# Kernel optimization log

Measured on AMD Instinct MI355X. Metric: run time of the kernel, lower is better.

The kernel has to match this reference:

```python
import jax, jax.numpy as jnp
import numpy as np

PAD_TOKEN = 0.0
REPLACEMENT_PROB = 0.1


def setup_inputs() -> dict:
    key = jax.random.key(0)
    # item-ID-like values in [0, 100000); zeros act as pad tokens
    x = jax.random.randint(key, (16384, 2048), 0, 100000).astype(jnp.float32)
    return {"x": x}


def reference(x):
    """Stochastic Swap Noise: replace ~p of non-pad positions with values
    sampled without replacement from the non-pad values of the tensor.

    Jit-friendly equivalent of torch's
      bernoulli -> masked_select compaction -> randperm -> scatter
    chain: a single argsort on random keys (pads keyed to +2.0) both
    compacts the non-pad values to the front AND shuffles them; a cumsum
    over the replacement mask assigns each replaced position its donor.
    """
    key = jax.random.key(42)
    k_bern, k_shuf = jax.random.split(key)

    nonpad = x != PAD_TOKEN                                        # [B,S] bool
    repl = (jax.random.uniform(k_bern, x.shape) < REPLACEMENT_PROB) & nonpad

    flat_x = x.reshape(-1)                                          # [N]
    flat_nonpad = nonpad.reshape(-1)
    flat_repl = repl.reshape(-1)

    # compaction + shuffle in one sort: non-pad elems get uniform [0,1) keys,
    # pads get 2.0 so they sink to the end.
    r = jnp.where(flat_nonpad, jax.random.uniform(k_shuf, flat_x.shape), 2.0)
    order = jnp.argsort(r)
    donors = flat_x[order]                                          # shuffled non-pad values first

    # k-th replaced position (in flat order) takes donors[k]
    rank = jnp.cumsum(flat_repl) - 1                                # -1 where not replaced (masked out below)
    out = jnp.where(flat_repl, donors[rank], flat_x)
    return out.reshape(x.shape)
```

## Files before the change

kernel.cpp:

```cpp
#include <hip/hip_runtime.h>
#include <stdint.h>

static __host__ __device__ inline uint32_t rotl32(uint32_t x, int r) {
#if defined(__HIP_DEVICE_COMPILE__)
  return __builtin_amdgcn_alignbit(x, x, (uint32_t)(32 - r));
#else
  return (x << r) | (x >> (32 - r));
#endif
}

static __host__ __device__ inline void tf2x32(uint32_t k0, uint32_t k1,
                                              uint32_t x0, uint32_t x1,
                                              uint32_t& o0, uint32_t& o1) {
  uint32_t k2 = k0 ^ k1 ^ 0x1BD11BDAu;
#define TFR(a) { x0 += x1; x1 = rotl32(x1, a); x1 ^= x0; }
  x0 += k0; x1 += k1;
  TFR(13) TFR(15) TFR(26) TFR(6)
  x0 += k1; x1 += k2 + 1u;
  TFR(17) TFR(29) TFR(16) TFR(24)
  x0 += k2; x1 += k0 + 2u;
  TFR(13) TFR(15) TFR(26) TFR(6)
  x0 += k0; x1 += k1 + 3u;
  TFR(17) TFR(29) TFR(16) TFR(24)
  x0 += k1; x1 += k2 + 4u;
  TFR(13) TFR(15) TFR(26) TFR(6)
  x0 += k2; x1 += k0 + 5u;
#undef TFR
  o0 = x0; o1 = x1;
}

static __device__ inline uint32_t fold_bits(uint32_t k0, uint32_t k1, uint32_t ctr) {
  uint32_t a, b;
  tf2x32(k0, k1, 0u, ctr, a, b);
  return a ^ b;
}

#define CUT2      917504u
#define NBINS2    1792u
#define NH        2048
#define ELEMS_G   8192
#define GPOOL     1216u
#define BSCAP     2432u
#define WIN       4096
#define CAPDUMP   3932160u
#define STRIDE    2432u
#define MASKI     0x07FFFFFFu
#define BERN_THR  838861u



template<bool BOUNDS>
__global__ __launch_bounds__(256) void k_gen(const float* __restrict__ x,
                                             uint64_t* __restrict__ mask,
                                             uint32_t* __restrict__ rsums,
                                             uint32_t* __restrict__ dumpCursor,
                                             uint2* __restrict__ dump,
                                             uint32_t bk0, uint32_t bk1,
                                             uint32_t sk0, uint32_t sk1, int n) {
  __shared__ uint2 pool[GPOOL];
  __shared__ uint32_t wcnt[4];
  __shared__ uint32_t lpoolCnt, lgbase;
  int tid = threadIdx.x, lane = tid & 63, wid = tid >> 6;
  int base = blockIdx.x * ELEMS_G;
  if (tid == 0) lpoolCnt = 0;
  __syncthreads();

  uint32_t cnt = 0;
  uint64_t lt = (1ull << lane) - 1ull;
  unsigned long long bball[4];
  for (int it = 0; it < ELEMS_G / 1024; it++) {
    int e0 = base + it * 1024 + wid * 256 + lane * 4;
    float4 xv;
    if (!BOUNDS || e0 + 3 < n) {
      xv = *reinterpret_cast<const float4*>(x + e0);
    } else {
      xv.x = (e0 + 0 < n) ? x[e0 + 0] : 0.0f;
      xv.y = (e0 + 1 < n) ? x[e0 + 1] : 0.0f;
      xv.z = (e0 + 2 < n) ? x[e0 + 2] : 0.0f;
      xv.w = (e0 + 3 < n) ? x[e0 + 3] : 0.0f;
    }
#define GENE(e, comp)                                                     \
    {                                                                     \
      uint32_t ii = (uint32_t)(e0 + e);                                   \
      bool np = (comp != 0.0f);                                           \
      uint32_t bb = fold_bits(bk0, bk1, ii);                              \
      bool rr = np && ((bb >> 9) < BERN_THR);                             \
      bball[e] = __ballot(rr);                                            \
      uint32_t mm = fold_bits(sk0, sk1, ii) >> 9;                         \
      bool cand = np && (mm < CUT2);                                      \
      unsigned long long cb = __ballot(cand);                             \
      uint32_t pb = 0;                                                    \
      if (lane == 0 && cb) pb = atomicAdd(&lpoolCnt, (uint32_t)__popcll(cb)); \
      pb = __builtin_amdgcn_readfirstlane(pb);                            \
      if (cand) {                                                         \
        uint32_t slot = pb + (uint32_t)__popcll(cb & lt);                 \
        if (slot < GPOOL) {                                               \
          uint32_t v = (uint32_t)comp;                                    \
          pool[slot] = make_uint2((mm << 12) | (v >> 5),                  \
                                  ((v & 31u) << 27) | ii);                \
        }                                                                 \
      }                                                                   \
    }
    GENE(0, xv.x) GENE(1, xv.y) GENE(2, xv.z) GENE(3, xv.w)
#undef GENE
    cnt += (uint32_t)(__popcll(bball[0]) + __popcll(bball[1]) +
                      __popcll(bball[2]) + __popcll(bball[3]));
    if (lane == 0) {
      uint32_t ci = (uint32_t)blockIdx.x * 32u + (uint32_t)it * 4u + (uint32_t)wid;
      if (!BOUNDS) {
        mask[ci * 4 + 0] = bball[0]; mask[ci * 4 + 1] = bball[1];
        mask[ci * 4 + 2] = bball[2]; mask[ci * 4 + 3] = bball[3];
      } else {
        for (int e = 0; e < 4; e++)
          if ((int)(ci * 256u + (uint32_t)e * 64u) < n) mask[ci * 4 + e] = bball[e];
      }
    }
  }
  if (lane == 0) wcnt[wid] = cnt;
  __syncthreads();
  if (tid == 0) {
    rsums[blockIdx.x] = wcnt[0] + wcnt[1] + wcnt[2] + wcnt[3];
    uint32_t pc = lpoolCnt; if (pc > GPOOL) pc = GPOOL;
    lgbase = atomicAdd((unsigned int*)dumpCursor, pc);
  }
  __syncthreads();
  uint32_t pc = lpoolCnt; if (pc > GPOOL) pc = GPOOL;
  uint32_t gb = lgbase;
  for (uint32_t j = tid; j < pc; j += 256) {
    uint32_t d = gb + j;
    if (d < CAPDUMP) dump[d] = pool[j];
  }
}

__global__ void k_scan2(uint32_t* __restrict__ data0, int n0,
                        uint32_t* __restrict__ data1, int n1) {
  __shared__ uint32_t wsum[4];
  uint32_t* data = (blockIdx.x == 0) ? data0 : data1;
  int n = (blockIdx.x == 0) ? n0 : n1;
  int tid = threadIdx.x, lane = tid & 63, wid = tid >> 6;
  uint32_t running = 0;
  for (int base = 0; base < n; base += 256) {
    int i = base + tid;
    uint32_t v = (i < n) ? data[i] : 0u;
    uint32_t incl = v;
    for (int d = 1; d < 64; d <<= 1) {
      uint32_t t = __shfl_up(incl, (unsigned)d, 64);
      if (lane >= d) incl += t;
    }
    if (lane == 63) wsum[wid] = incl;
    __syncthreads();
    uint32_t woff = 0, tot = 0;
    for (int w = 0; w < 4; w++) { uint32_t s = wsum[w]; if (w < wid) woff += s; tot += s; }
    if (i < n) data[i] = running + woff + (incl - v);
    running += tot;
    __syncthreads();
  }
  if (tid == 0) data[n] = running;
}

__global__ __launch_bounds__(256) void k_regroup(const uint2* __restrict__ dump,
                                                 const uint32_t* __restrict__ dumpCursor,
                                                 uint32_t* __restrict__ fineCursor,
                                                 uint2* __restrict__ fine) {
  __shared__ uint2    pool2[WIN];
  __shared__ uint32_t lhist[NH];
  __shared__ uint32_t lgbase[NH];
  __shared__ uint32_t wsums[4];
  int tid = threadIdx.x, lane = tid & 63, wid = tid >> 6;
  uint32_t total = dumpCursor[0];
  if (total > CAPDUMP) total = CAPDUMP;
  uint32_t wbase = blockIdx.x * (uint32_t)WIN;
  if (wbase >= total) return;
  uint32_t valid = total - wbase;
  if (valid > WIN) valid = WIN;

  for (int b = tid; b < NH; b += 256) lhist[b] = 0;
  __syncthreads();
  uint2 e[WIN / 256];
#pragma unroll
  for (int q = 0; q < WIN / 256; q++) {
    uint32_t j = (uint32_t)q * 256u + (uint32_t)tid;
    e[q] = (j < valid) ? dump[wbase + j] : make_uint2(0u, 0u);
    if (j < valid) atomicAdd(&lhist[e[q].x >> 21], 1u);
  }
  __syncthreads();
  for (int b = tid; b < NH; b += 256) {
    uint32_t h = lhist[b];
    lgbase[b] = h ? atomicAdd((unsigned int*)&fineCursor[b], h) : 0u;
  }
  __syncthreads();
  uint32_t hv[8], tsum = 0;
#pragma unroll
  for (int j = 0; j < 8; j++) { hv[j] = lhist[8 * tid + j]; tsum += hv[j]; }
  uint32_t incl = tsum;
  for (int d = 1; d < 64; d <<= 1) {
    uint32_t t = __shfl_up(incl, (unsigned)d, 64);
    if (lane >= d) incl += t;
  }
  if (lane == 63) wsums[wid] = incl;
  __syncthreads();
  if (wid == 0) {
    uint32_t v = (lane < 4) ? wsums[lane] : 0u;
    uint32_t in2 = v;
    for (int d = 1; d < 4; d <<= 1) {
      uint32_t t = __shfl_up(in2, (unsigned)d, 64);
      if (lane >= d) in2 += t;
    }
    if (lane < 4) wsums[lane] = in2 - v;
  }
  __syncthreads();
  uint32_t run = wsums[wid] + (incl - tsum);
#pragma unroll
  for (int j = 0; j < 8; j++) { uint32_t h = hv[j]; lhist[8 * tid + j] = run; run += h; }
  __syncthreads();
#pragma unroll
  for (int q = 0; q < WIN / 256; q++) {
    uint32_t j = (uint32_t)q * 256u + (uint32_t)tid;
    if (j < valid) {
      uint32_t b = e[q].x >> 21;
      uint32_t lpos = atomicAdd(&lhist[b], 1u);
      pool2[lpos] = e[q];
    }
  }
  __syncthreads();
  for (uint32_t j = tid; j < valid; j += 256) {
    uint2 p = pool2[j];
    uint32_t b = p.x >> 21;
    uint32_t st = (b == 0) ? 0u : lhist[b - 1];
    uint32_t dst = lgbase[b] + (j - st);
    if (dst < STRIDE) fine[(size_t)b * STRIDE + dst] = p;
  }
}

__global__ __launch_bounds__(256) void k_binsort(const uint2* __restrict__ pairs,
                                                 const uint32_t* __restrict__ binPrefix,
                                                 float* __restrict__ donors) {
  __shared__ uint2    lbuf[BSCAP];
  __shared__ uint32_t hist[512];
  __shared__ uint32_t wsums[4];
  int tid = threadIdx.x, lane = tid & 63, wid = tid >> 6;
  uint32_t bin = blockIdx.x;
  uint32_t gbase = binPrefix[bin];
  uint32_t cnt = binPrefix[bin + 1] - gbase;
  if (cnt > STRIDE) cnt = STRIDE;
  if (cnt > BSCAP) cnt = BSCAP;
  const uint2* src = pairs + (size_t)bin * STRIDE;

  for (int c = tid; c < 512; c += 256) hist[c] = 0;
  __syncthreads();
  for (uint32_t j = tid; j < cnt; j += 256)
    atomicAdd(&hist[(src[j].x >> 12) & 511u], 1u);
  __syncthreads();
  uint32_t h0 = hist[2 * tid], h1 = hist[2 * tid + 1];
  uint32_t tsum = h0 + h1;
  uint32_t incl = tsum;
  for (int d = 1; d < 64; d <<= 1) {
    uint32_t t = __shfl_up(incl, (unsigned)d, 64);
    if (lane >= d) incl += t;
  }
  if (lane == 63) wsums[wid] = incl;
  __syncthreads();
  if (wid == 0) {
    uint32_t v = (lane < 4) ? wsums[lane] : 0u;
    uint32_t in2 = v;
    for (int d = 1; d < 4; d <<= 1) {
      uint32_t t = __shfl_up(in2, (unsigned)d, 64);
      if (lane >= d) in2 += t;
    }
    if (lane < 4) wsums[lane] = in2 - v;
  }
  __syncthreads();
  uint32_t texcl = wsums[wid] + (incl - tsum);
  uint32_t e0 = texcl, e1 = e0 + h0;
  __syncthreads();
  hist[2 * tid] = e0; hist[2 * tid + 1] = e1;
  __syncthreads();
  for (uint32_t j = tid; j < cnt; j += 256) {
    uint2 p = src[j];
    uint32_t c = (p.x >> 12) & 511u;
    uint32_t lpos = atomicAdd(&hist[c], 1u);
    lbuf[lpos] = p;
  }
  __syncthreads();
  for (int c = tid; c < 512; c += 256) {
    uint32_t lo = (c == 0) ? 0u : hist[c - 1];
    uint32_t hi = hist[c];
    for (uint32_t u = lo + 1; u < hi; u++) {
      uint2 v = lbuf[u];
      uint32_t w = u;
      while (w > lo && (lbuf[w - 1].y & MASKI) > (v.y & MASKI)) {
        lbuf[w] = lbuf[w - 1];
        w--;
      }
      lbuf[w] = v;
    }
  }
  __syncthreads();
  for (uint32_t j = tid; j < cnt; j += 256) {
    uint2 p = lbuf[j];
    uint32_t v = ((p.x & 0xFFFu) << 5) | (p.y >> 27);
    donors[gbase + j] = (float)v;
  }
}

template<bool BOUNDS>
__global__ __launch_bounds__(256) void k_final(const float* __restrict__ x,
                                               const uint64_t* __restrict__ mask,
                                               const uint32_t* __restrict__ rsums,
                                               const float* __restrict__ donors,
                                               float* __restrict__ out, int n) {
  __shared__ uint64_t lw[ELEMS_G / 64];
  __shared__ uint32_t ctot[32], cpre[32];
  int tid = threadIdx.x, lane = tid & 63, wid = tid >> 6;
  int base = blockIdx.x * ELEMS_G;
  int wordBase = blockIdx.x * (ELEMS_G / 64);
  if (tid < ELEMS_G / 64) {
    uint64_t w = 0ull;
    int wI = wordBase + tid;
    if (!BOUNDS || (((wI >> 2) * 256) + ((wI & 3) * 64) < n)) w = mask[wI];
    lw[tid] = w;
  }
  __syncthreads();
  if (tid < 32) {
    ctot[tid] = (uint32_t)(__popcll(lw[4 * tid]) + __popcll(lw[4 * tid + 1]) +
                           __popcll(lw[4 * tid + 2]) + __popcll(lw[4 * tid + 3]));
  }
  __syncthreads();
  if (tid == 0) {
    uint32_t run = 0;
    for (int c = 0; c < 32; c++) { cpre[c] = run; run += ctot[c]; }
  }
  __syncthreads();
  uint32_t rbase = rsums[blockIdx.x];
  uint64_t lt = (1ull << lane) - 1ull;
  for (int it = 0; it < ELEMS_G / 1024; it++) {
    int c = it * 4 + wid;
    uint64_t b0 = lw[c * 4 + 0], b1 = lw[c * 4 + 1],
             b2 = lw[c * 4 + 2], b3 = lw[c * 4 + 3];
    uint32_t running = rbase + cpre[c];
    int e0 = base + it * 1024 + wid * 256 + lane * 4;
    uint32_t below = (uint32_t)(__popcll(b0 & lt) + __popcll(b1 & lt) +
                                __popcll(b2 & lt) + __popcll(b3 & lt));
    uint32_t r0 = (uint32_t)((b0 >> lane) & 1ull), r1 = (uint32_t)((b1 >> lane) & 1ull);
    uint32_t r2 = (uint32_t)((b2 >> lane) & 1ull), r3 = (uint32_t)((b3 >> lane) & 1ull);
    uint32_t rk = running + below;
    float4 xv;
    if (!BOUNDS || e0 + 3 < n) {
      xv = *reinterpret_cast<const float4*>(x + e0);
    } else {
      xv.x = (e0 + 0 < n) ? x[e0 + 0] : 0.0f;
      xv.y = (e0 + 1 < n) ? x[e0 + 1] : 0.0f;
      xv.z = (e0 + 2 < n) ? x[e0 + 2] : 0.0f;
      xv.w = (e0 + 3 < n) ? x[e0 + 3] : 0.0f;
    }
    float4 ov;
    ov.x = r0 ? donors[rk] : xv.x;               rk += r0;
    ov.y = r1 ? donors[rk] : xv.y;               rk += r1;
    ov.z = r2 ? donors[rk] : xv.z;               rk += r2;
    ov.w = r3 ? donors[rk] : xv.w;
    if (!BOUNDS || e0 + 3 < n) {
      *reinterpret_cast<float4*>(out + e0) = ov;
    } else {
      if (e0 + 0 < n) out[e0 + 0] = ov.x;
      if (e0 + 1 < n) out[e0 + 1] = ov.y;
      if (e0 + 2 < n) out[e0 + 2] = ov.z;
      if (e0 + 3 < n) out[e0 + 3] = ov.w;
    }
  }
}

extern "C" void kernel_launch(void* const* d_in, const int* in_sizes, int n_in,
                              void* d_out, int out_size, void* d_ws, size_t ws_size,
                              hipStream_t stream) {
  const float* x = (const float*)d_in[0];
  float* out = (float*)d_out;
  int n = in_sizes[0];
  (void)n_in; (void)out_size; (void)ws_size;

  uint32_t bk0, bk1, sk0, sk1;
  tf2x32(0u, 42u, 0u, 0u, bk0, bk1);
  tf2x32(0u, 42u, 0u, 1u, sk0, sk1);

  int nBlkG = (n + ELEMS_G - 1) / ELEMS_G;
  bool exact = ((n % ELEMS_G) == 0);

  size_t off = 0;
  auto alloc = [&](size_t bytes) -> void* {
    void* p = (uint8_t*)d_ws + off;
    off += (bytes + 255) & ~(size_t)255;
    return p;
  };
  uint32_t* dumpCursor = (uint32_t*)alloc(4);
  uint32_t* fineCursor = (uint32_t*)alloc((size_t)(NH + 1) * 4);
  size_t zeroBytes = off;
  uint32_t* rsums      = (uint32_t*)alloc((size_t)(nBlkG + 1) * 4);
  uint64_t* mask       = (uint64_t*)alloc((size_t)((n + 63) / 64 + 4) * 8);
  uint2*    dump       = (uint2*)alloc((size_t)CAPDUMP * 8);
  uint2*    fine       = (uint2*)alloc((size_t)NBINS2 * STRIDE * 8);
  float*    donors     = (float*)dump;

  hipMemsetAsync(d_ws, 0, zeroBytes, stream);

  if (exact)
    k_gen<false><<<nBlkG, 256, 0, stream>>>(x, mask, rsums, dumpCursor, dump,
                                            bk0, bk1, sk0, sk1, n);
  else
    k_gen<true><<<nBlkG, 256, 0, stream>>>(x, mask, rsums, dumpCursor, dump,
                                           bk0, bk1, sk0, sk1, n);
  int nWin = (int)((CAPDUMP + WIN - 1) / WIN);
  k_regroup<<<nWin, 256, 0, stream>>>(dump, dumpCursor, fineCursor, fine);
  k_scan2<<<2, 256, 0, stream>>>(rsums, nBlkG, fineCursor, (int)NBINS2);
  k_binsort<<<(int)NBINS2, 256, 0, stream>>>(fine, fineCursor, donors);
  if (exact)
    k_final<false><<<nBlkG, 256, 0, stream>>>(x, mask, rsums, donors, out, n);
  else
    k_final<true><<<nBlkG, 256, 0, stream>>>(x, mask, rsums, donors, out, n);
}
```

Before: 334.9 us.

## Split generation kernel and replace single-pass regroup with two-level coarse/fine scatter

The fused generation kernel is split into a Bernoulli-mask kernel and a candidate-pool kernel, each reading x separately. The single regroup pass over 2048 buckets, with its large shared histogram and global atomics per bucket, is replaced by a two-level radix scatter: 56 coarse buckets first, then 32 fine buckets per coarse bucket. This cuts shared-memory histogram and scan work per block and should make the scattered writes more coalesced. In exchange it adds an extra read of x, an extra full pass through global memory, and two more launches.

```diff
diff --git a/kernel.cpp b/kernel.cpp
--- a/kernel.cpp
+++ b/kernel.cpp
@@ -36,37 +36,30 @@
 }
 
 #define CUT2      917504u
-#define NBINS2    1792u
-#define NH        2048
+#define NCOARSE   56u
+#define CSTRIDE   69632u
+#define WPC       17u
+#define NFINE     1792u
+#define STRIDE    2432u
+#define BSCAP     2432u
 #define ELEMS_G   8192
 #define GPOOL     1216u
-#define BSCAP     2432u
 #define WIN       4096
 #define CAPDUMP   3932160u
-#define STRIDE    2432u
 #define MASKI     0x07FFFFFFu
 #define BERN_THR  838861u
 
 
 
 template<bool BOUNDS>
-__global__ __launch_bounds__(256) void k_gen(const float* __restrict__ x,
-                                             uint64_t* __restrict__ mask,
-                                             uint32_t* __restrict__ rsums,
-                                             uint32_t* __restrict__ dumpCursor,
-                                             uint2* __restrict__ dump,
-                                             uint32_t bk0, uint32_t bk1,
-                                             uint32_t sk0, uint32_t sk1, int n) {
-  __shared__ uint2 pool[GPOOL];
+__global__ __launch_bounds__(256) void k_bern(const float* __restrict__ x,
+                                              uint64_t* __restrict__ mask,
+                                              uint32_t* __restrict__ rsums,
+                                              uint32_t bk0, uint32_t bk1, int n) {
   __shared__ uint32_t wcnt[4];
-  __shared__ uint32_t lpoolCnt, lgbase;
   int tid = threadIdx.x, lane = tid & 63, wid = tid >> 6;
   int base = blockIdx.x * ELEMS_G;
-  if (tid == 0) lpoolCnt = 0;
-  __syncthreads();
-
   uint32_t cnt = 0;
-  uint64_t lt = (1ull << lane) - 1ull;
   unsigned long long bball[4];
   for (int it = 0; it < ELEMS_G / 1024; it++) {
     int e0 = base + it * 1024 + wid * 256 + lane * 4;
@@ -79,15 +72,61 @@
       xv.z = (e0 + 2 < n) ? x[e0 + 2] : 0.0f;
       xv.w = (e0 + 3 < n) ? x[e0 + 3] : 0.0f;
     }
-#define GENE(e, comp)                                                     \
+#define BERNE(e, comp)                                                    \
     {                                                                     \
       uint32_t ii = (uint32_t)(e0 + e);                                   \
-      bool np = (comp != 0.0f);                                           \
       uint32_t bb = fold_bits(bk0, bk1, ii);                              \
-      bool rr = np && ((bb >> 9) < BERN_THR);                             \
+      bool rr = (comp != 0.0f) && ((bb >> 9) < BERN_THR);                 \
       bball[e] = __ballot(rr);                                            \
+    }
+    BERNE(0, xv.x) BERNE(1, xv.y) BERNE(2, xv.z) BERNE(3, xv.w)
+#undef BERNE
+    cnt += (uint32_t)(__popcll(bball[0]) + __popcll(bball[1]) +
+                      __popcll(bball[2]) + __popcll(bball[3]));
+    if (lane == 0) {
+      uint32_t ci = (uint32_t)blockIdx.x * 32u + (uint32_t)it * 4u + (uint32_t)wid;
+      if (!BOUNDS) {
+        mask[ci * 4 + 0] = bball[0]; mask[ci * 4 + 1] = bball[1];
+        mask[ci * 4 + 2] = bball[2]; mask[ci * 4 + 3] = bball[3];
+      } else {
+        for (int e = 0; e < 4; e++)
+          if ((int)(ci * 256u + (uint32_t)e * 64u) < n) mask[ci * 4 + e] = bball[e];
+      }
+    }
+  }
+  if (lane == 0) wcnt[wid] = cnt;
+  __syncthreads();
+  if (tid == 0) rsums[blockIdx.x] = wcnt[0] + wcnt[1] + wcnt[2] + wcnt[3];
+}
+
+template<bool BOUNDS>
+__global__ __launch_bounds__(256) void k_cand(const float* __restrict__ x,
+                                              uint32_t* __restrict__ dumpCursor,
+                                              uint2* __restrict__ dump,
+                                              uint32_t sk0, uint32_t sk1, int n) {
+  __shared__ uint2 pool[GPOOL];
+  __shared__ uint32_t lpoolCnt, lgbase;
+  int tid = threadIdx.x, lane = tid & 63, wid = tid >> 6;
+  int base = blockIdx.x * ELEMS_G;
+  if (tid == 0) lpoolCnt = 0;
+  __syncthreads();
+  uint64_t lt = (1ull << lane) - 1ull;
+  for (int it = 0; it < ELEMS_G / 1024; it++) {
+    int e0 = base + it * 1024 + wid * 256 + lane * 4;
+    float4 xv;
+    if (!BOUNDS || e0 + 3 < n) {
+      xv = *reinterpret_cast<const float4*>(x + e0);
+    } else {
+      xv.x = (e0 + 0 < n) ? x[e0 + 0] : 0.0f;
+      xv.y = (e0 + 1 < n) ? x[e0 + 1] : 0.0f;
+      xv.z = (e0 + 2 < n) ? x[e0 + 2] : 0.0f;
+      xv.w = (e0 + 3 < n) ? x[e0 + 3] : 0.0f;
+    }
+#define CANDE(e, comp)                                                    \
+    {                                                                     \
+      uint32_t ii = (uint32_t)(e0 + e);                                   \
       uint32_t mm = fold_bits(sk0, sk1, ii) >> 9;                         \
-      bool cand = np && (mm < CUT2);                                      \
+      bool cand = (comp != 0.0f) && (mm < CUT2);                          \
       unsigned long long cb = __ballot(cand);                             \
       uint32_t pb = 0;                                                    \
       if (lane == 0 && cb) pb = atomicAdd(&lpoolCnt, (uint32_t)__popcll(cb)); \
@@ -101,25 +140,11 @@
         }                                                                 \
       }                                                                   \
     }
-    GENE(0, xv.x) GENE(1, xv.y) GENE(2, xv.z) GENE(3, xv.w)
-#undef GENE
-    cnt += (uint32_t)(__popcll(bball[0]) + __popcll(bball[1]) +
-                      __popcll(bball[2]) + __popcll(bball[3]));
-    if (lane == 0) {
-      uint32_t ci = (uint32_t)blockIdx.x * 32u + (uint32_t)it * 4u + (uint32_t)wid;
-      if (!BOUNDS) {
-        mask[ci * 4 + 0] = bball[0]; mask[ci * 4 + 1] = bball[1];
-        mask[ci * 4 + 2] = bball[2]; mask[ci * 4 + 3] = bball[3];
-      } else {
-        for (int e = 0; e < 4; e++)
-          if ((int)(ci * 256u + (uint32_t)e * 64u) < n) mask[ci * 4 + e] = bball[e];
-      }
-    }
-  }
-  if (lane == 0) wcnt[wid] = cnt;
+    CANDE(0, xv.x) CANDE(1, xv.y) CANDE(2, xv.z) CANDE(3, xv.w)
+#undef CANDE
+  }
   __syncthreads();
   if (tid == 0) {
-    rsums[blockIdx.x] = wcnt[0] + wcnt[1] + wcnt[2] + wcnt[3];
     uint32_t pc = lpoolCnt; if (pc > GPOOL) pc = GPOOL;
     lgbase = atomicAdd((unsigned int*)dumpCursor, pc);
   }
@@ -158,77 +183,118 @@
   if (tid == 0) data[n] = running;
 }
 
-__global__ __launch_bounds__(256) void k_regroup(const uint2* __restrict__ dump,
-                                                 const uint32_t* __restrict__ dumpCursor,
-                                                 uint32_t* __restrict__ fineCursor,
-                                                 uint2* __restrict__ fine) {
-  __shared__ uint2    pool2[WIN];
-  __shared__ uint32_t lhist[NH];
-  __shared__ uint32_t lgbase[NH];
-  __shared__ uint32_t wsums[4];
-  int tid = threadIdx.x, lane = tid & 63, wid = tid >> 6;
-  uint32_t total = dumpCursor[0];
-  if (total > CAPDUMP) total = CAPDUMP;
+__global__ __launch_bounds__(256) void k_regA(const uint2* __restrict__ dump,
+                                              const uint32_t* __restrict__ dumpCursor,
+                                              uint32_t* __restrict__ coarseCursor,
+                                              uint2* __restrict__ coarse) {
+  __shared__ uint2 pool2[WIN];
+  __shared__ uint32_t lh[4][64];
+  __shared__ uint32_t hbase[64], lgb[64], lcur[64];
+  int tid = threadIdx.x, lane = tid & 63, wid = tid >> 6;
+  uint32_t total = dumpCursor[0]; if (total > CAPDUMP) total = CAPDUMP;
   uint32_t wbase = blockIdx.x * (uint32_t)WIN;
   if (wbase >= total) return;
-  uint32_t valid = total - wbase;
-  if (valid > WIN) valid = WIN;
-
-  for (int b = tid; b < NH; b += 256) lhist[b] = 0;
+  uint32_t valid = total - wbase; if (valid > WIN) valid = WIN;
+  lh[wid][lane] = 0;
   __syncthreads();
   uint2 e[WIN / 256];
 #pragma unroll
   for (int q = 0; q < WIN / 256; q++) {
     uint32_t j = (uint32_t)q * 256u + (uint32_t)tid;
     e[q] = (j < valid) ? dump[wbase + j] : make_uint2(0u, 0u);
-    if (j < valid) atomicAdd(&lhist[e[q].x >> 21], 1u);
-  }
-  __syncthreads();
-  for (int b = tid; b < NH; b += 256) {
-    uint32_t h = lhist[b];
-    lgbase[b] = h ? atomicAdd((unsigned int*)&fineCursor[b], h) : 0u;
-  }
-  __syncthreads();
-  uint32_t hv[8], tsum = 0;
-#pragma unroll
-  for (int j = 0; j < 8; j++) { hv[j] = lhist[8 * tid + j]; tsum += hv[j]; }
-  uint32_t incl = tsum;
-  for (int d = 1; d < 64; d <<= 1) {
-    uint32_t t = __shfl_up(incl, (unsigned)d, 64);
-    if (lane >= d) incl += t;
-  }
-  if (lane == 63) wsums[wid] = incl;
+    if (j < valid) atomicAdd(&lh[wid][e[q].x >> 26], 1u);
+  }
+  __syncthreads();
+  if (tid < 64) {
+    uint32_t h = lh[0][tid] + lh[1][tid] + lh[2][tid] + lh[3][tid];
+    lgb[tid] = (h && tid < NCOARSE) ? atomicAdd((unsigned int*)&coarseCursor[tid], h) : 0u;
+    lcur[tid] = h;
+  }
   __syncthreads();
   if (wid == 0) {
-    uint32_t v = (lane < 4) ? wsums[lane] : 0u;
-    uint32_t in2 = v;
-    for (int d = 1; d < 4; d <<= 1) {
-      uint32_t t = __shfl_up(in2, (unsigned)d, 64);
-      if (lane >= d) in2 += t;
-    }
-    if (lane < 4) wsums[lane] = in2 - v;
-  }
-  __syncthreads();
-  uint32_t run = wsums[wid] + (incl - tsum);
-#pragma unroll
-  for (int j = 0; j < 8; j++) { uint32_t h = hv[j]; lhist[8 * tid + j] = run; run += h; }
+    uint32_t v = lcur[lane];
+    uint32_t incl = v;
+    for (int d = 1; d < 64; d <<= 1) {
+      uint32_t t = __shfl_up(incl, (unsigned)d, 64);
+      if (lane >= d) incl += t;
+    }
+    hbase[lane] = incl - v;
+    lcur[lane] = incl - v;
+  }
   __syncthreads();
 #pragma unroll
   for (int q = 0; q < WIN / 256; q++) {
     uint32_t j = (uint32_t)q * 256u + (uint32_t)tid;
     if (j < valid) {
-      uint32_t b = e[q].x >> 21;
-      uint32_t lpos = atomicAdd(&lhist[b], 1u);
+      uint32_t c = e[q].x >> 26;
+      uint32_t lpos = atomicAdd(&lcur[c], 1u);
       pool2[lpos] = e[q];
     }
   }
   __syncthreads();
   for (uint32_t j = tid; j < valid; j += 256) {
     uint2 p = pool2[j];
-    uint32_t b = p.x >> 21;
-    uint32_t st = (b == 0) ? 0u : lhist[b - 1];
-    uint32_t dst = lgbase[b] + (j - st);
-    if (dst < STRIDE) fine[(size_t)b * STRIDE + dst] = p;
+    uint32_t c = p.x >> 26;
+    uint32_t dst = lgb[c] + (j - hbase[c]);
+    if (dst < CSTRIDE) coarse[(size_t)c * CSTRIDE + dst] = p;
+  }
+}
+
+__global__ __launch_bounds__(256) void k_regB(const uint2* __restrict__ coarse,
+                                              const uint32_t* __restrict__ coarseCursor,
+                                              uint32_t* __restrict__ fineCursor,
+                                              uint2* __restrict__ fine) {
+  __shared__ uint2 pool2[WIN];
+  __shared__ uint32_t lh[4][32];
+  __shared__ uint32_t hbase[32], lgb[32], lcur[32];
+  int tid = threadIdx.x, lane = tid & 63, wid = tid >> 6;
+  uint32_t c = blockIdx.x / WPC, w = blockIdx.x % WPC;
+  uint32_t ccnt = coarseCursor[c]; if (ccnt > CSTRIDE) ccnt = CSTRIDE;
+  uint32_t wbase = w * (uint32_t)WIN;
+  if (wbase >= ccnt) return;
+  uint32_t valid = ccnt - wbase; if (valid > WIN) valid = WIN;
+  const uint2* src = coarse + (size_t)c * CSTRIDE + wbase;
+  if (tid < 128) lh[tid >> 5][tid & 31] = 0;
+  __syncthreads();
+  uint2 e[WIN / 256];
+#pragma unroll
+  for (int q = 0; q < WIN / 256; q++) {
+    uint32_t j = (uint32_t)q * 256u + (uint32_t)tid;
+    e[q] = (j < valid) ? src[j] : make_uint2(0u, 0u);
+    if (j < valid) atomicAdd(&lh[wid][(e[q].x >> 21) & 31u], 1u);
+  }
+  __syncthreads();
+  if (tid < 32) {
+    uint32_t h = lh[0][tid] + lh[1][tid] + lh[2][tid] + lh[3][tid];
+    lgb[tid] = h ? atomicAdd((unsigned int*)&fineCursor[c * 32u + tid], h) : 0u;
+    lcur[tid] = h;
+  }
+  __syncthreads();
+  if (wid == 0) {
+    uint32_t v = (lane < 32) ? lcur[lane] : 0u;
+    uint32_t incl = v;
+    for (int d = 1; d < 32; d <<= 1) {
+      uint32_t t = __shfl_up(incl, (unsigned)d, 64);
+      if (lane >= d) incl += t;
+    }
+    if (lane < 32) { hbase[lane] = incl - v; lcur[lane] = incl - v; }
+  }
+  __syncthreads();
+#pragma unroll
+  for (int q = 0; q < WIN / 256; q++) {
+    uint32_t j = (uint32_t)q * 256u + (uint32_t)tid;
+    if (j < valid) {
+      uint32_t f = (e[q].x >> 21) & 31u;
+      uint32_t lpos = atomicAdd(&lcur[f], 1u);
+      pool2[lpos] = e[q];
+    }
+  }
+  __syncthreads();
+  for (uint32_t j = tid; j < valid; j += 256) {
+    uint2 p = pool2[j];
+    uint32_t f = (p.x >> 21) & 31u;
+    uint32_t dst = lgb[f] + (j - hbase[f]);
+    if (dst < STRIDE) fine[(size_t)(c * 32u + f) * STRIDE + dst] = p;
   }
 }
 
@@ -390,27 +456,33 @@
     off += (bytes + 255) & ~(size_t)255;
     return p;
   };
-  uint32_t* dumpCursor = (uint32_t*)alloc(4);
-  uint32_t* fineCursor = (uint32_t*)alloc((size_t)(NH + 1) * 4);
+  uint32_t* dumpCursor   = (uint32_t*)alloc(4);
+  uint32_t* coarseCursor = (uint32_t*)alloc((size_t)64 * 4);
+  uint32_t* fineCursor   = (uint32_t*)alloc((size_t)(NFINE + 1) * 4);
   size_t zeroBytes = off;
-  uint32_t* rsums      = (uint32_t*)alloc((size_t)(nBlkG + 1) * 4);
-  uint64_t* mask       = (uint64_t*)alloc((size_t)((n + 63) / 64 + 4) * 8);
-  uint2*    dump       = (uint2*)alloc((size_t)CAPDUMP * 8);
-  uint2*    fine       = (uint2*)alloc((size_t)NBINS2 * STRIDE * 8);
-  float*    donors     = (float*)dump;
+  uint32_t* rsums = (uint32_t*)alloc((size_t)(nBlkG + 1) * 4);
+  uint64_t* mask  = (uint64_t*)alloc((size_t)((n + 63) / 64 + 4) * 8);
+  uint2* bufA = (uint2*)alloc((size_t)NFINE * STRIDE * 8);
+  uint2* bufB = (uint2*)alloc((size_t)NCOARSE * CSTRIDE * 8);
+  uint2* dump = bufA;
+  uint2* coarse = bufB;
+  uint2* fine = bufA;
+  float* donors = (float*)bufB;
 
   hipMemsetAsync(d_ws, 0, zeroBytes, stream);
 
-  if (exact)
-    k_gen<false><<<nBlkG, 256, 0, stream>>>(x, mask, rsums, dumpCursor, dump,
-                                            bk0, bk1, sk0, sk1, n);
-  else
-    k_gen<true><<<nBlkG, 256, 0, stream>>>(x, mask, rsums, dumpCursor, dump,
-                                           bk0, bk1, sk0, sk1, n);
-  int nWin = (int)((CAPDUMP + WIN - 1) / WIN);
-  k_regroup<<<nWin, 256, 0, stream>>>(dump, dumpCursor, fineCursor, fine);
-  k_scan2<<<2, 256, 0, stream>>>(rsums, nBlkG, fineCursor, (int)NBINS2);
-  k_binsort<<<(int)NBINS2, 256, 0, stream>>>(fine, fineCursor, donors);
+  if (exact) {
+    k_bern<false><<<nBlkG, 256, 0, stream>>>(x, mask, rsums, bk0, bk1, n);
+    k_cand<false><<<nBlkG, 256, 0, stream>>>(x, dumpCursor, dump, sk0, sk1, n);
+  } else {
+    k_bern<true><<<nBlkG, 256, 0, stream>>>(x, mask, rsums, bk0, bk1, n);
+    k_cand<true><<<nBlkG, 256, 0, stream>>>(x, dumpCursor, dump, sk0, sk1, n);
+  }
+  int nWinA = (int)(CAPDUMP / WIN);
+  k_regA<<<nWinA, 256, 0, stream>>>(dump, dumpCursor, coarseCursor, coarse);
+  k_regB<<<(int)(NCOARSE * WPC), 256, 0, stream>>>(coarse, coarseCursor, fineCursor, fine);
+  k_scan2<<<2, 256, 0, stream>>>(rsums, nBlkG, fineCursor, (int)NFINE);
+  k_binsort<<<(int)NFINE, 256, 0, stream>>>(fine, fineCursor, donors);
   if (exact)
     k_final<false><<<nBlkG, 256, 0, stream>>>(x, mask, rsums, donors, out, n);
   else
```

Result: no change. 330.0 us (-1.5%).
